# Performance work log

Hardware: AMD Instinct MI355X
Metric: run time of the kernel (lower is better)

Reference implementation:

```python
import jax, jax.numpy as jnp
import numpy as np

B, T, E = 2, 2048, 1024
NEXP, TOPK, INTER = 8, 2, 1408


def setup_inputs() -> dict:
    key = jax.random.key(0)
    ks = jax.random.split(key, 5)
    s = 0.02
    return {
        "x": jax.random.normal(ks[0], (B, T, E), dtype=jnp.float32),
        "gate_w": jax.random.normal(ks[1], (NEXP, E), dtype=jnp.float32) * s,
        "wg": jax.random.normal(ks[2], (NEXP, INTER, E), dtype=jnp.float32) * s,
        "wu": jax.random.normal(ks[3], (NEXP, INTER, E), dtype=jnp.float32) * s,
        "wd": jax.random.normal(ks[4], (NEXP, E, INTER), dtype=jnp.float32) * s,
    }


def reference(x, gate_w, wg, wu, wd):
    # Router: scores [B,T,NEXP], topk softmax over selected experts only
    scores = jnp.einsum("btd,ed->bte", x, gate_w)
    topk_scores, topk_idx = jax.lax.top_k(scores, TOPK)  # [B,T,K]
    topk_probs = jax.nn.softmax(topk_scores, axis=-1)
    # Scatter back to dense gating probs [B,T,NEXP] (topk indices are unique)
    onehot = jax.nn.one_hot(topk_idx, NEXP, dtype=x.dtype)  # [B,T,K,NEXP]
    gating = jnp.sum(onehot * topk_probs[..., None], axis=-2)  # [B,T,NEXP]
    # Dense compute-all-experts (faithful to the original module)
    g = jnp.einsum("btd,eid->btei", x, wg)  # [B,T,NEXP,INTER]
    u = jnp.einsum("btd,eid->btei", x, wu)
    h = jax.nn.silu(g) * u
    expert_out = jnp.einsum("btei,edi->bted", h, wd)  # [B,T,NEXP,E]
    y = jnp.sum(gating[..., None] * expert_out, axis=-2)  # [B,T,E]
    return y
```

## Files before the change

kernel.cpp:

```cpp
#include <hip/hip_runtime.h>
#include <hip/hip_bf16.h>
#include <stdint.h>

typedef __hip_bfloat16 bf16;
typedef __attribute__((ext_vector_type(8))) short short8;
typedef __attribute__((ext_vector_type(4))) float f32x4;

#define NTOK  4096
#define EDIM  1024
#define NEXPT 8
#define INTERD 1408
#define MAXP  4096
#define WELEM (NEXPT * INTERD * EDIM)

#define GL16(g, l) __builtin_amdgcn_global_load_lds( \
    (const __attribute__((address_space(1))) unsigned int*)(g), \
    (__attribute__((address_space(3))) unsigned int*)(l), 16, 0, 0)

#define WAIT_VM(n)   asm volatile("s_waitcnt vmcnt(" #n ")" ::: "memory")
#define BAR()        __builtin_amdgcn_s_barrier()
#define PRIO(n)      __builtin_amdgcn_s_setprio(n)

__global__ __launch_bounds__(256) void prep_kernel(const float* __restrict__ wg, bf16* __restrict__ wgb,
                                                   const float* __restrict__ wu, bf16* __restrict__ wub,
                                                   const float* __restrict__ wd, bf16* __restrict__ wdb,
                                                   const float* __restrict__ x,
                                                   const float* __restrict__ gw,
                                                   bf16* __restrict__ xb,
                                                   int* __restrict__ sel,
                                                   float* __restrict__ tprob) {
    int b = blockIdx.x;
    if (b < 3072) {
        const float* src; bf16* dst;
        if (b < 1024)      { src = wg; dst = wgb; }
        else if (b < 2048) { src = wu; dst = wub; b -= 1024; }
        else               { src = wd; dst = wdb; b -= 2048; }
        int i = (b * 256 + threadIdx.x) * 4;
        int stride = 1024 * 256 * 4;
        for (; i < WELEM; i += stride) {
            float4 v = *(const float4*)(src + i);
            ushort4 o; bf16 t;
            t = __float2bfloat16(v.x); o.x = *(unsigned short*)&t;
            t = __float2bfloat16(v.y); o.y = *(unsigned short*)&t;
            t = __float2bfloat16(v.z); o.z = *(unsigned short*)&t;
            t = __float2bfloat16(v.w); o.w = *(unsigned short*)&t;
            *(ushort4*)(dst + i) = o;
        }
        return;
    }
    int t = (b - 3072) * 4 + (threadIdx.x >> 6);
    int lane = threadIdx.x & 63;
    const float* xr = x + (size_t)t * EDIM;
    float xv[16];
#pragma unroll
    for (int j = 0; j < 4; j++) {
        float4 v = *(const float4*)(xr + lane * 16 + j * 4);
        xv[4 * j] = v.x; xv[4 * j + 1] = v.y; xv[4 * j + 2] = v.z; xv[4 * j + 3] = v.w;
    }
    bf16* xbr = xb + (size_t)t * EDIM;
#pragma unroll
    for (int j = 0; j < 4; j++) {
        ushort4 o; bf16 c;
        c = __float2bfloat16(xv[4 * j]);     o.x = *(unsigned short*)&c;
        c = __float2bfloat16(xv[4 * j + 1]); o.y = *(unsigned short*)&c;
        c = __float2bfloat16(xv[4 * j + 2]); o.z = *(unsigned short*)&c;
        c = __float2bfloat16(xv[4 * j + 3]); o.w = *(unsigned short*)&c;
        *(ushort4*)(xbr + lane * 16 + j * 4) = o;
    }
    double acc[NEXPT];
#pragma unroll
    for (int e = 0; e < NEXPT; e++) acc[e] = 0.0;
#pragma unroll
    for (int e = 0; e < NEXPT; e++) {
        const float* gr = gw + e * EDIM + lane * 16;
#pragma unroll
        for (int j = 0; j < 16; j++) acc[e] += (double)xv[j] * (double)gr[j];
    }
#pragma unroll
    for (int off = 32; off >= 1; off >>= 1) {
#pragma unroll
        for (int e = 0; e < NEXPT; e++) acc[e] += __shfl_xor(acc[e], off, 64);
    }
    if (lane == 0) {
        int e0 = 0; double s0 = acc[0];
        for (int e = 1; e < NEXPT; e++) if (acc[e] > s0) { s0 = acc[e]; e0 = e; }
        int e1 = -1; double s1 = -1e300;
        for (int e = 0; e < NEXPT; e++) if (e != e0 && acc[e] > s1) { s1 = acc[e]; e1 = e; }
        float z = __expf((float)(s1 - s0));
        float p0 = 1.f / (1.f + z);
        sel[t] = e0 | (e1 << 8);
        tprob[2 * t] = p0;
        tprob[2 * t + 1] = 1.f - p0;
    }
}

__global__ __launch_bounds__(512) void bucket_kernel(const int* __restrict__ sel,
                                                     const float* __restrict__ tprob,
                                                     int* __restrict__ counts,
                                                     int* __restrict__ offsets,
                                                     int* __restrict__ ptok,
                                                     float* __restrict__ pprob,
                                                     int* __restrict__ wq1,
                                                     int* __restrict__ wq2) {
    __shared__ int scnt[NEXPT];
    int w = threadIdx.x >> 6;
    int lane = threadIdx.x & 63;
    unsigned long long ltmask = (lane == 63) ? ~0ull >> 1 : (1ull << lane) - 1;
    int base = 0;
    for (int t0 = 0; t0 < NTOK; t0 += 64) {
        int t = t0 + lane;
        int s = sel[t];
        int e0 = s & 0xff, e1 = (s >> 8) & 0xff;
        unsigned long long m0 = __ballot(e0 == w);
        if (e0 == w) {
            int pos = base + __popcll(m0 & ltmask);
            ptok[w * MAXP + pos] = t;
            pprob[w * MAXP + pos] = tprob[2 * t];
        }
        base += __popcll(m0);
        unsigned long long m1 = __ballot(e1 == w);
        if (e1 == w) {
            int pos = base + __popcll(m1 & ltmask);
            ptok[w * MAXP + pos] = t;
            pprob[w * MAXP + pos] = tprob[2 * t + 1];
        }
        base += __popcll(m1);
    }
    if (lane == 0) scnt[w] = base;
    __syncthreads();
    if (threadIdx.x < NEXPT) {
        int off = 0;
        for (int e = 0; e < (int)threadIdx.x; e++) off += scnt[e];
        counts[threadIdx.x] = scnt[threadIdx.x];
        offsets[threadIdx.x] = off;
        wq1[threadIdx.x * 32] = 0;
        wq2[threadIdx.x * 32] = 0;
    }
}

__global__ __launch_bounds__(512, 4) void gemm1_kernel(const bf16* __restrict__ xb,
                                                       const bf16* __restrict__ wgb,
                                                       const bf16* __restrict__ wub,
                                                       bf16* __restrict__ hout,
                                                       const int* __restrict__ counts,
                                                       const int* __restrict__ offsets,
                                                       const int* __restrict__ ptok,
                                                       const float* __restrict__ pprob,
                                                       int* __restrict__ wq1) {
    int eown = blockIdx.x & 7;

    __shared__ __align__(16) bf16 smem[3 * 12288];
    __shared__ int s_wi;

    int tid  = threadIdx.x;
    int lane = tid & 63;
    int wid  = tid >> 6;
    int wm   = wid >> 2;
    int wn   = wid & 3;

    int srow = tid >> 2;
    int qs   = (((tid & 3) ^ ((srow >> 1) & 3)) * 8);
    int l15  = lane & 15;
    int l4   = lane >> 4;

    int offA[4], offG[2];
#pragma unroll
    for (int m = 0; m < 4; m++) {
        int r = wm * 64 + m * 16 + l15;
        offA[m] = r * 32 + ((l4 ^ ((r >> 1) & 3)) * 8);
    }
#pragma unroll
    for (int n = 0; n < 2; n++) {
        int r = wn * 32 + n * 16 + l15;
        offG[n] = r * 32 + ((l4 ^ ((r >> 1) & 3)) * 8);
    }

    for (int ei = 0; ei < NEXPT; ++ei) {
        int e = (eown + ei) & 7;
        int cnt = counts[e];
        int mtiles = (cnt + 127) >> 7;
        int tiles = mtiles * (INTERD / 128);
        int hbase = offsets[e];

        for (;;) {
            if (tid == 0) s_wi = atomicAdd(&wq1[e * 32], 1);
            __syncthreads();
            int wi = s_wi;
            __syncthreads();
            if (wi >= tiles) break;
            int mt = wi % mtiles;
            int nt = wi / mtiles;
            int m0 = mt * 128;
            int n0 = nt * 128;

            WAIT_VM(0);
            const bf16* gA = xb + (size_t)ptok[e * MAXP + min(m0 + srow, cnt - 1)] * EDIM + qs;
            const bf16* gG = wgb + ((size_t)e * INTERD + n0 + srow) * EDIM + qs;
            const bf16* gU = wub + ((size_t)e * INTERD + n0 + srow) * EDIM + qs;

            f32x4 accg[4][2], accu[4][2];
#pragma unroll
            for (int m = 0; m < 4; m++)
#pragma unroll
                for (int n = 0; n < 2; n++) {
                    accg[m][n] = (f32x4){0.f, 0.f, 0.f, 0.f};
                    accu[m][n] = (f32x4){0.f, 0.f, 0.f, 0.f};
                }

#define SB1(t) (smem + ((t) % 3) * 12288)
#define G1_STAGE(t) do { bf16* sb_ = SB1(t); int ko_ = (t) * 32; \
            GL16(gA + ko_, sb_ + wid * 512); \
            GL16(gG + ko_, sb_ + 4096 + wid * 512); \
            GL16(gU + ko_, sb_ + 8192 + wid * 512); } while (0)

            G1_STAGE(0); G1_STAGE(1);

            for (int t = 0; t < 32; ++t) {
                if (t < 30)       { G1_STAGE(t + 2); WAIT_VM(6); }
                else if (t == 30) { WAIT_VM(3); }
                else              { WAIT_VM(0); }
                BAR();
                const bf16* sb = SB1(t);
                short8 a_[4], gf[2], uf[2];
#pragma unroll
                for (int m = 0; m < 4; m++) a_[m] = *(const short8*)&sb[offA[m]];
#pragma unroll
                for (int n = 0; n < 2; n++) {
                    gf[n] = *(const short8*)&sb[4096 + offG[n]];
                    uf[n] = *(const short8*)&sb[8192 + offG[n]];
                }
                PRIO(1);
#pragma unroll
                for (int m = 0; m < 4; m++)
#pragma unroll
                    for (int n = 0; n < 2; n++) {
                        accg[m][n] = __builtin_amdgcn_mfma_f32_16x16x32_bf16(a_[m], gf[n], accg[m][n], 0, 0, 0);
                        accu[m][n] = __builtin_amdgcn_mfma_f32_16x16x32_bf16(a_[m], uf[n], accu[m][n], 0, 0, 0);
                    }
                PRIO(0);
                BAR();
            }
#undef SB1
#undef G1_STAGE

#pragma unroll
            for (int m = 0; m < 4; m++)
#pragma unroll
                for (int n = 0; n < 2; n++)
#pragma unroll
                    for (int r = 0; r < 4; r++) {
                        int pos = m0 + wm * 64 + m * 16 + l4 * 4 + r;
                        if (pos < cnt) {
                            int col = n0 + wn * 32 + n * 16 + l15;
                            float p = pprob[e * MAXP + pos];
                            float gv = accg[m][n][r];
                            float uv = accu[m][n][r];
                            float hv = (gv / (1.f + __expf(-gv))) * uv * p;
                            hout[(size_t)(hbase + pos) * INTERD + col] = __float2bfloat16(hv);
                        }
                    }
        }
    }
}

__global__ __launch_bounds__(512, 4) void gemm2_kernel(const bf16* __restrict__ h,
                                                       const bf16* __restrict__ wdb,
                                                       float* __restrict__ y,
                                                       const int* __restrict__ counts,
                                                       const int* __restrict__ offsets,
                                                       const int* __restrict__ ptok,
                                                       int* __restrict__ wq2) {
    int eown = blockIdx.x & 7;

    __shared__ __align__(16) bf16 smem[2 * 16384];
    __shared__ int s_wi;

    int tid  = threadIdx.x;
    int lane = tid & 63;
    int wid  = tid >> 6;
    int wm   = wid >> 2;
    int wn   = wid & 3;

    int srow = tid >> 3;
    int qs   = (((tid & 7) ^ (srow & 7)) * 8);
    int l15  = lane & 15;
    int l4   = lane >> 4;

    int offA[4][2], offB[2][2];
#pragma unroll
    for (int m = 0; m < 4; m++) {
        int r = wm * 64 + m * 16 + l15;
#pragma unroll
        for (int kh = 0; kh < 2; kh++)
            offA[m][kh] = r * 64 + (((kh * 4 + l4) ^ (r & 7)) * 8);
    }
#pragma unroll
    for (int n = 0; n < 2; n++) {
        int r = wn * 32 + n * 16 + l15;
#pragma unroll
        for (int kh = 0; kh < 2; kh++)
            offB[n][kh] = 8192 + r * 64 + (((kh * 4 + l4) ^ (r & 7)) * 8);
    }

    for (int ei = 0; ei < NEXPT; ++ei) {
        int e = (eown + ei) & 7;
        int cnt = counts[e];
        int mtiles = (cnt + 127) >> 7;
        int tiles = mtiles * (EDIM / 128);
        int hbase = offsets[e];

        for (;;) {
            if (tid == 0) s_wi = atomicAdd(&wq2[e * 32], 1);
            __syncthreads();
            int wi = s_wi;
            __syncthreads();
            if (wi >= tiles) break;
            int mt = wi % mtiles;
            int nt = wi / mtiles;
            int m0 = mt * 128;
            int n0 = nt * 128;

            WAIT_VM(0);
            const bf16* gA0 = h + (size_t)(hbase + min(m0 + srow,      cnt - 1)) * INTERD + qs;
            const bf16* gA1 = h + (size_t)(hbase + min(m0 + 64 + srow, cnt - 1)) * INTERD + qs;
            const bf16* gB0 = wdb + ((size_t)e * EDIM + n0 + srow) * INTERD + qs;
            const bf16* gB1 = wdb + ((size_t)e * EDIM + n0 + 64 + srow) * INTERD + qs;

            f32x4 acc[4][2];
#pragma unroll
            for (int m = 0; m < 4; m++)
#pragma unroll
                for (int n = 0; n < 2; n++) acc[m][n] = (f32x4){0.f, 0.f, 0.f, 0.f};

#define SB2(t) (smem + ((t) & 1) * 16384)
#define G2_STAGE(t) do { bf16* sb_ = SB2(t); int ko_ = (t) * 64; \
            GL16(gA0 + ko_, sb_ + wid * 512); \
            GL16(gA1 + ko_, sb_ + 4096 + wid * 512); \
            GL16(gB0 + ko_, sb_ + 8192 + wid * 512); \
            GL16(gB1 + ko_, sb_ + 12288 + wid * 512); } while (0)

            G2_STAGE(0);

            for (int t = 0; t < 22; ++t) {
                if (t < 21) { G2_STAGE(t + 1); WAIT_VM(4); }
                else        { WAIT_VM(0); }
                BAR();
                const bf16* sb = SB2(t);
                short8 a_[4][2], b_[2][2];
#pragma unroll
                for (int m = 0; m < 4; m++)
#pragma unroll
                    for (int kh = 0; kh < 2; kh++)
                        a_[m][kh] = *(const short8*)&sb[offA[m][kh]];
#pragma unroll
                for (int n = 0; n < 2; n++)
#pragma unroll
                    for (int kh = 0; kh < 2; kh++)
                        b_[n][kh] = *(const short8*)&sb[offB[n][kh]];
                PRIO(1);
#pragma unroll
                for (int m = 0; m < 4; m++)
#pragma unroll
                    for (int n = 0; n < 2; n++)
#pragma unroll
                        for (int kh = 0; kh < 2; kh++)
                            acc[m][n] = __builtin_amdgcn_mfma_f32_16x16x32_bf16(
                                a_[m][kh], b_[n][kh], acc[m][n], 0, 0, 0);
                PRIO(0);
                BAR();
            }
#undef SB2
#undef G2_STAGE

#pragma unroll
            for (int m = 0; m < 4; m++) {
                int pos = m0 + wm * 64 + m * 16 + l4 * 4;
                int tok[4];
#pragma unroll
                for (int r = 0; r < 4; r++)
                    tok[r] = (pos + r < cnt) ? ptok[e * MAXP + pos + r] : -1;
#pragma unroll
                for (int n = 0; n < 2; n++) {
                    int col = n0 + wn * 32 + n * 16 + l15;
#pragma unroll
                    for (int r = 0; r < 4; r++)
                        if (tok[r] >= 0)
                            atomicAdd(&y[(size_t)tok[r] * EDIM + col], acc[m][n][r]);
                }
            }
        }
    }
}

extern "C" void kernel_launch(void* const* d_in, const int* in_sizes, int n_in,
                              void* d_out, int out_size, void* d_ws, size_t ws_size,
                              hipStream_t stream) {
    const float* x      = (const float*)d_in[0];
    const float* gate_w = (const float*)d_in[1];
    const float* wg     = (const float*)d_in[2];
    const float* wu     = (const float*)d_in[3];
    const float* wd     = (const float*)d_in[4];
    float* y = (float*)d_out;

    char* ws = (char*)d_ws;
    constexpr size_t SZ_XB = (size_t)NTOK * EDIM * 2;
    constexpr size_t SZ_W  = (size_t)WELEM * 2;
    constexpr size_t SZ_H  = (size_t)NTOK * 2 * INTERD * 2;
    bf16* xb  = (bf16*)ws;
    bf16* wgb = (bf16*)(ws + SZ_XB);
    bf16* wub = (bf16*)(ws + SZ_XB + SZ_W);
    bf16* wdb = (bf16*)(ws + SZ_XB + 2 * SZ_W);
    bf16* h   = (bf16*)(ws + SZ_XB + 3 * SZ_W);
    char* meta = ws + SZ_XB + 3 * SZ_W + SZ_H;
    int*   counts  = (int*)meta;
    int*   offsets = (int*)(meta + 256);
    int*   ptok    = (int*)(meta + 512);
    float* pprob   = (float*)(meta + 512 + (size_t)NEXPT * MAXP * 4);
    char*  meta2   = meta + 512 + (size_t)NEXPT * MAXP * 8;
    int*   wq1     = (int*)meta2;
    int*   wq2     = (int*)(meta2 + 1024);
    int*   sel     = (int*)(meta2 + 2048);
    float* tprob   = (float*)(meta2 + 2048 + (size_t)NTOK * 4);

    hipMemsetAsync(d_out, 0, (size_t)out_size * 4, stream);

    prep_kernel<<<3072 + NTOK / 4, 256, 0, stream>>>(wg, wgb, wu, wub, wd, wdb,
                                                     x, gate_w, xb, sel, tprob);
    bucket_kernel<<<1, 512, 0, stream>>>(sel, tprob, counts, offsets, ptok, pprob,
                                         wq1, wq2);

    gemm1_kernel<<<512, 512, 0, stream>>>(
        xb, wgb, wub, h, counts, offsets, ptok, pprob, wq1);
    gemm2_kernel<<<512, 512, 0, stream>>>(
        h, wdb, y, counts, offsets, ptok, wq2);
}
```

Before: 239.8 us.

## Replace gemm2 atomic scatter with bf16 staging buffer and gather combine kernel

gemm2 now writes its per-expert rows as bf16 into a staging buffer that reuses the wg bf16 region, instead of doing atomicAdd into y. The bucket kernel records an inverse map from each token-slot pair to its expert position. A new combine kernel gathers each token's two rows and sums them into y, so the output memset and the float atomics go away. The cost is an extra launch, an extra round trip through memory, and bf16 rounding of the expert outputs before the sum.

```diff
diff --git a/kernel.cpp b/kernel.cpp
--- a/kernel.cpp
+++ b/kernel.cpp
@@ -100,6 +100,7 @@
                                                      int* __restrict__ offsets,
                                                      int* __restrict__ ptok,
                                                      float* __restrict__ pprob,
+                                                     int* __restrict__ inv,
                                                      int* __restrict__ wq1,
                                                      int* __restrict__ wq2) {
     __shared__ int scnt[NEXPT];
@@ -116,6 +117,7 @@
             int pos = base + __popcll(m0 & ltmask);
             ptok[w * MAXP + pos] = t;
             pprob[w * MAXP + pos] = tprob[2 * t];
+            inv[2 * t] = (w << 16) | pos;
         }
         base += __popcll(m0);
         unsigned long long m1 = __ballot(e1 == w);
@@ -123,6 +125,7 @@
             int pos = base + __popcll(m1 & ltmask);
             ptok[w * MAXP + pos] = t;
             pprob[w * MAXP + pos] = tprob[2 * t + 1];
+            inv[2 * t + 1] = (w << 16) | pos;
         }
         base += __popcll(m1);
     }
@@ -265,10 +268,9 @@
 
 __global__ __launch_bounds__(512, 4) void gemm2_kernel(const bf16* __restrict__ h,
                                                        const bf16* __restrict__ wdb,
-                                                       float* __restrict__ y,
+                                                       bf16* __restrict__ out2,
                                                        const int* __restrict__ counts,
                                                        const int* __restrict__ offsets,
-                                                       const int* __restrict__ ptok,
                                                        int* __restrict__ wq2) {
     int eown = blockIdx.x & 7;
 
@@ -373,23 +375,41 @@
 #undef G2_STAGE
 
 #pragma unroll
-            for (int m = 0; m < 4; m++) {
-                int pos = m0 + wm * 64 + m * 16 + l4 * 4;
-                int tok[4];
-#pragma unroll
-                for (int r = 0; r < 4; r++)
-                    tok[r] = (pos + r < cnt) ? ptok[e * MAXP + pos + r] : -1;
-#pragma unroll
-                for (int n = 0; n < 2; n++) {
-                    int col = n0 + wn * 32 + n * 16 + l15;
-#pragma unroll
-                    for (int r = 0; r < 4; r++)
-                        if (tok[r] >= 0)
-                            atomicAdd(&y[(size_t)tok[r] * EDIM + col], acc[m][n][r]);
-                }
-            }
+            for (int m = 0; m < 4; m++)
+#pragma unroll
+                for (int n = 0; n < 2; n++)
+#pragma unroll
+                    for (int r = 0; r < 4; r++) {
+                        int pos = m0 + wm * 64 + m * 16 + l4 * 4 + r;
+                        if (pos < cnt) {
+                            int col = n0 + wn * 32 + n * 16 + l15;
+                            out2[(size_t)(hbase + pos) * EDIM + col] = __float2bfloat16(acc[m][n][r]);
+                        }
+                    }
         }
     }
+}
+
+__global__ __launch_bounds__(256) void combine_kernel(const bf16* __restrict__ out2,
+                                                      const int* __restrict__ inv,
+                                                      const int* __restrict__ offsets,
+                                                      float* __restrict__ y) {
+    int idx = blockIdx.x * 256 + threadIdx.x;
+    int t = idx >> 7;
+    int c = (idx & 127) * 8;
+    int a = inv[2 * t], b = inv[2 * t + 1];
+    const short8 va = *(const short8*)(out2 + (size_t)(offsets[a >> 16] + (a & 0xFFFF)) * EDIM + c);
+    const short8 vb = *(const short8*)(out2 + (size_t)(offsets[b >> 16] + (b & 0xFFFF)) * EDIM + c);
+    float o[8];
+#pragma unroll
+    for (int j = 0; j < 8; j++) {
+        unsigned ua = ((unsigned)(unsigned short)va[j]) << 16;
+        unsigned ub = ((unsigned)(unsigned short)vb[j]) << 16;
+        o[j] = *(float*)&ua + *(float*)&ub;
+    }
+    float* yp = y + (size_t)t * EDIM + c;
+    *(float4*)yp       = (float4){o[0], o[1], o[2], o[3]};
+    *(float4*)(yp + 4) = (float4){o[4], o[5], o[6], o[7]};
 }
 
 extern "C" void kernel_launch(void* const* d_in, const int* in_sizes, int n_in,
@@ -416,21 +436,22 @@
     int*   offsets = (int*)(meta + 256);
     int*   ptok    = (int*)(meta + 512);
     float* pprob   = (float*)(meta + 512 + (size_t)NEXPT * MAXP * 4);
-    char*  meta2   = meta + 512 + (size_t)NEXPT * MAXP * 8;
+    int*   inv     = (int*)(meta + 512 + (size_t)NEXPT * MAXP * 8);
+    char*  meta2   = meta + 512 + (size_t)NEXPT * MAXP * 8 + (size_t)NTOK * 2 * 4;
     int*   wq1     = (int*)meta2;
     int*   wq2     = (int*)(meta2 + 1024);
     int*   sel     = (int*)(meta2 + 2048);
     float* tprob   = (float*)(meta2 + 2048 + (size_t)NTOK * 4);
-
-    hipMemsetAsync(d_out, 0, (size_t)out_size * 4, stream);
+    bf16* out2 = (bf16*)(ws + SZ_XB);
 
     prep_kernel<<<3072 + NTOK / 4, 256, 0, stream>>>(wg, wgb, wu, wub, wd, wdb,
                                                      x, gate_w, xb, sel, tprob);
-    bucket_kernel<<<1, 512, 0, stream>>>(sel, tprob, counts, offsets, ptok, pprob,
+    bucket_kernel<<<1, 512, 0, stream>>>(sel, tprob, counts, offsets, ptok, pprob, inv,
                                          wq1, wq2);
 
     gemm1_kernel<<<512, 512, 0, stream>>>(
         xb, wgb, wub, h, counts, offsets, ptok, pprob, wq1);
     gemm2_kernel<<<512, 512, 0, stream>>>(
-        h, wdb, y, counts, offsets, ptok, wq2);
-}
+        h, wdb, out2, counts, offsets, wq2);
+    combine_kernel<<<NTOK * EDIM / 8 / 256, 256, 0, stream>>>(out2, inv, offsets, y);
+}
```

Result: faster. 219.6 us (-8.4%).
